# Performance work log

Hardware: AMD Instinct MI355X
Metric: run time of the kernel (lower is better)

## Reference

```python
import jax, jax.numpy as jnp
import numpy as np

TQ, T, D = 2048, 16384, 256
H, KD, VD, DOUT = 8, 32, 32, 256


def setup_inputs() -> dict:
    key = jax.random.key(0)
    ks = jax.random.split(key, 8)
    w_scale = 1.0 / np.sqrt(D)
    return {
        "query": jax.random.normal(ks[0], (TQ, D), dtype=jnp.float32),
        "key": jax.random.normal(ks[1], (T, D), dtype=jnp.float32),
        "value": jax.random.normal(ks[2], (T, D), dtype=jnp.float32),
        "wq": jax.random.normal(ks[3], (D, H * KD), dtype=jnp.float32) * w_scale,
        "bq": jnp.zeros((H * KD,), dtype=jnp.float32),
        "wk": jax.random.normal(ks[4], (D, H * KD), dtype=jnp.float32) * w_scale,
        "bk": jnp.zeros((H * KD,), dtype=jnp.float32),
        "wv": jax.random.normal(ks[5], (D, H * VD), dtype=jnp.float32) * w_scale,
        "bv": jnp.zeros((H * VD,), dtype=jnp.float32),
        "wo": jax.random.normal(ks[6], (H * VD, DOUT), dtype=jnp.float32) * (1.0 / np.sqrt(H * VD)),
        "bo": jnp.zeros((DOUT,), dtype=jnp.float32),
    }


def reference(query, key, value, wq, bq, wk, bk, wv, bv, wo, bo):
    # Linear projections to heads: [Tq,H,KD], [T,H,KD], [T,H,VD]
    qh = (query @ wq + bq).reshape(TQ, H, KD)
    kh = (key @ wk + bk).reshape(T, H, KD)
    vh = (value @ wv + bv).reshape(T, H, VD)
    # Chunked online-softmax attention == exact softmax attention.
    # Query scaled by 1/sqrt(head_dim) as in the memory-efficient impl.
    scale = np.float32(1.0 / np.sqrt(KD))
    logits = jnp.einsum("qhd,khd->hqk", qh * scale, kh)  # [H,Tq,T]
    weights = jax.nn.softmax(logits, axis=-1)
    attn = jnp.einsum("hqk,khd->qhd", weights, vh).reshape(TQ, H * VD)
    return attn @ wo + bo  # [Tq, DOUT]
```

## Files before the change

### kernel.cpp

```cpp
#include <hip/hip_runtime.h>
#include <stdint.h>


typedef float f32x4 __attribute__((ext_vector_type(4)));
typedef __bf16 bf16x8 __attribute__((ext_vector_type(8)));

__device__ __forceinline__ unsigned short f2bf(float f) {
  unsigned int u = __builtin_bit_cast(unsigned int, f);
  u += 0x7FFFu + ((u >> 16) & 1u);
  return (unsigned short)(u >> 16);
}
__device__ __forceinline__ float bf2f(unsigned u) {
  return __builtin_bit_cast(float, u << 16);
}
__device__ __forceinline__ f32x4 mfma16(bf16x8 a, bf16x8 b, f32x4 c) {
  return __builtin_amdgcn_mfma_f32_16x16x32_bf16(a, b, c, 0, 0, 0);
}
__device__ __forceinline__ float ex2(float x) {
#if __has_builtin(__builtin_amdgcn_exp2f)
  return __builtin_amdgcn_exp2f(x);
#else
  return exp2f(x);
#endif
}
__device__ __forceinline__ uint2 pack4(f32x4 a) {
  uint2 r;
  r.x = (unsigned)f2bf(a[0]) | ((unsigned)f2bf(a[1]) << 16);
  r.y = (unsigned)f2bf(a[2]) | ((unsigned)f2bf(a[3]) << 16);
  return r;
}

#define QSCALE 0.25503483f

__global__ __launch_bounds__(256) void convert_w_kernel(
    const float* __restrict__ wq, const float* __restrict__ wk,
    const float* __restrict__ wv, const float* __restrict__ wo,
    unsigned short* __restrict__ tq, unsigned short* __restrict__ tk,
    unsigned short* __restrict__ tv, unsigned short* __restrict__ to)
{
  const int mat = blockIdx.x >> 6, k0 = (blockIdx.x & 63) * 4, n = threadIdx.x;
  const float* src; unsigned short* dst;
  if (mat == 0) { src = wq; dst = tq; }
  else if (mat == 1) { src = wk; dst = tk; }
  else if (mat == 2) { src = wv; dst = tv; }
  else { src = wo; dst = to; }
  unsigned e0 = f2bf(src[(size_t)(k0 + 0) * 256 + n]);
  unsigned e1 = f2bf(src[(size_t)(k0 + 1) * 256 + n]);
  unsigned e2 = f2bf(src[(size_t)(k0 + 2) * 256 + n]);
  unsigned e3 = f2bf(src[(size_t)(k0 + 3) * 256 + n]);
  uint2 pk = { e0 | (e1 << 16), e2 | (e3 << 16) };
  *(uint2*)&dst[(size_t)n * 256 + k0] = pk;
}

__global__ __launch_bounds__(512) void proj4_kernel(
    const float* __restrict__ Xq, const float* __restrict__ Xk,
    const float* __restrict__ Xv,
    const unsigned short* __restrict__ Wtq, const unsigned short* __restrict__ Wtk,
    const unsigned short* __restrict__ Wtv,
    const float* __restrict__ Bq, const float* __restrict__ Bk,
    const float* __restrict__ Bv,
    unsigned short* __restrict__ Oq, unsigned short* __restrict__ Ok,
    unsigned short* __restrict__ Ov)
{
  const int mat = blockIdx.y;
  const float* X; const unsigned short* Wt; const float* Bp; unsigned short* Op;
  int N; float scale; int vmode;
  if (mat == 0) {
    if (blockIdx.x >= 32) return;
    X = Xq; Wt = Wtq; Bp = Bq; Op = Oq; N = 2048; scale = QSCALE; vmode = 0;
  } else if (mat == 1) {
    X = Xk; Wt = Wtk; Bp = Bk; Op = Ok; N = 16384; scale = 1.f; vmode = 0;
  } else {
    X = Xv; Wt = Wtv; Bp = Bv; Op = Ov; N = 16384; scale = 1.f; vmode = 1;
  }
  const int tid = threadIdx.x;
  const int w = tid >> 6, lane = tid & 63, g = lane >> 4, c = lane & 15;
  const int m0 = blockIdx.x * 64;

  __shared__ __align__(16) unsigned short Xs[64 * 40];
  __shared__ __align__(16) unsigned short Ws[256 * 40];

  const f32x4 zero4 = {0.f, 0.f, 0.f, 0.f};
  f32x4 acc[4][2];
  #pragma unroll
  for (int i = 0; i < 4; ++i) { acc[i][0] = zero4; acc[i][1] = zero4; }

  const int xrow = tid >> 3, xseg = (tid & 7) * 4;
  const int wrow = tid >> 1, wseg = (tid & 1) * 16;

  for (int k0 = 0; k0 < 256; k0 += 32) {
    if (k0) __syncthreads();
    {
      float4 x = *(const float4*)&X[(size_t)(m0 + xrow) * 256 + k0 + xseg];
      uint2 px = { (unsigned)f2bf(x.x) | ((unsigned)f2bf(x.y) << 16),
                   (unsigned)f2bf(x.z) | ((unsigned)f2bf(x.w) << 16) };
      *(uint2*)&Xs[xrow * 40 + xseg] = px;
    }
    {
      const unsigned short* wp = Wt + (size_t)wrow * 256 + k0 + wseg;
      int4 w0 = *(const int4*)wp;
      int4 w1 = *(const int4*)(wp + 8);
      *(int4*)&Ws[wrow * 40 + wseg] = w0;
      *(int4*)&Ws[wrow * 40 + wseg + 8] = w1;
    }
    __syncthreads();

    bf16x8 a[4], b[2];
    #pragma unroll
    for (int rt = 0; rt < 4; ++rt)
      a[rt] = *(const bf16x8*)&Xs[(16 * rt + c) * 40 + 8 * g];
    #pragma unroll
    for (int ct = 0; ct < 2; ++ct)
      b[ct] = *(const bf16x8*)&Ws[(32 * w + 16 * ct + c) * 40 + 8 * g];
    #pragma unroll
    for (int rt = 0; rt < 4; ++rt)
      #pragma unroll
      for (int ct = 0; ct < 2; ++ct)
        acc[rt][ct] = mfma16(a[rt], b[ct], acc[rt][ct]);
  }

  #pragma unroll
  for (int ct = 0; ct < 2; ++ct) {
    const int col = 32 * w + 16 * ct + c;
    const float bv = Bp[col];
    const int hh = col >> 5, d = col & 31;
    #pragma unroll
    for (int rt = 0; rt < 4; ++rt)
      #pragma unroll
      for (int r = 0; r < 4; ++r) {
        const int row = m0 + 16 * rt + 4 * g + r;
        const unsigned short v = f2bf((acc[rt][ct][r] + bv) * scale);
        if (vmode) {
          const int pr = (row & ~31) | (((row >> 3) & 1) << 4) |
                         (((row >> 2) & 1) << 3) | (((row >> 4) & 1) << 2) |
                         (row & 3);
          Op[((size_t)hh * 32 + d) * (size_t)N + pr] = v;
        } else {
          Op[((size_t)hh * N + row) * 32 + d] = v;
        }
      }
  }
}

__global__ __launch_bounds__(256) void attn4_kernel(
    const unsigned short* __restrict__ qh, const unsigned short* __restrict__ kh,
    const unsigned short* __restrict__ vth,
    unsigned short* __restrict__ part_o, float* __restrict__ part_l)
{
  const int f = blockIdx.x + 16 * (blockIdx.y + 8 * blockIdx.z);
  const int v = (f & 7) * 128 + (f >> 3);
  const int qb = v & 15, h = (v >> 4) & 7, sp = v >> 7;

  const int tid = threadIdx.x;
  const int w = tid >> 6, lane = tid & 63, g = lane >> 4, c = lane & 15;
  const int q0 = qb * 128 + w * 32;

  __shared__ __align__(16) unsigned short Ks[2][64 * 40];
  __shared__ __align__(16) unsigned short Vt[2][32 * 72];

  const bf16x8 qf0 = *(const bf16x8*)&qh[((size_t)h * 2048 + q0 + c) * 32 + 8 * g];
  const bf16x8 qf1 = *(const bf16x8*)&qh[((size_t)h * 2048 + q0 + 16 + c) * 32 + 8 * g];

  const f32x4 zero4 = {0.f, 0.f, 0.f, 0.f};
  f32x4 acc00 = zero4, acc01 = zero4, acc10 = zero4, acc11 = zero4;
  float l0 = 0.f, l1 = 0.f;

  const int skey = tid >> 2, sseg = (tid & 3) * 8;
  const int kwoff = skey * 40 + sseg;
  const int vrow = tid >> 3, vseg = (tid & 7) * 8;
  const int vwoff = vrow * 72 + vseg;

  const unsigned short* kp = kh + (size_t)h * 524288 +
                             ((size_t)(sp * 2048) + skey) * 32 + sseg;
  const unsigned short* vp = vth + ((size_t)h * 32 + vrow) * 16384 +
                             sp * 2048 + vseg;

  int4 kA = *(const int4*)kp;
  int4 vA = *(const int4*)vp;
  *(int4*)&Ks[0][kwoff] = kA;
  *(int4*)&Vt[0][vwoff] = vA;
  kA = *(const int4*)(kp + 2048);
  vA = *(const int4*)(vp + 64);
  __syncthreads();

  for (int it = 0; it < 32; ++it) {
    const int cur = it & 1;
    if (it < 31) {
      *(int4*)&Ks[cur ^ 1][kwoff] = kA;
      *(int4*)&Vt[cur ^ 1][vwoff] = vA;
      const int t2 = (it + 2) & 31;
      kA = *(const int4*)(kp + t2 * 2048);
      vA = *(const int4*)(vp + t2 * 64);
    }

    const unsigned short* Kb = &Ks[cur][0];
    const unsigned short* Vb = &Vt[cur][0];
    bf16x8 kf0 = *(const bf16x8*)&Kb[(c) * 40 + 8 * g];
    bf16x8 kf1 = *(const bf16x8*)&Kb[(16 + c) * 40 + 8 * g];
    bf16x8 kf2 = *(const bf16x8*)&Kb[(32 + c) * 40 + 8 * g];
    bf16x8 kf3 = *(const bf16x8*)&Kb[(48 + c) * 40 + 8 * g];

    f32x4 s0 = mfma16(kf0, qf0, zero4);
    f32x4 s1 = mfma16(kf1, qf0, zero4);
    f32x4 s2 = mfma16(kf2, qf0, zero4);
    f32x4 s3 = mfma16(kf3, qf0, zero4);
    union { __bf16 b[8]; bf16x8 v; } pa00, pa01, pa10, pa11;
    float rs0 = 0.f;
    #pragma unroll
    for (int r = 0; r < 4; ++r) {
      float p0 = ex2(s0[r]), p1 = ex2(s1[r]);
      float p2 = ex2(s2[r]), p3 = ex2(s3[r]);
      rs0 += (p0 + p1) + (p2 + p3);
      pa00.b[r] = (__bf16)p0; pa00.b[4 + r] = (__bf16)p1;
      pa01.b[r] = (__bf16)p2; pa01.b[4 + r] = (__bf16)p3;
    }
    rs0 += __shfl_xor(rs0, 16);
    rs0 += __shfl_xor(rs0, 32);
    l0 += rs0;
    s0 = mfma16(kf0, qf1, zero4);
    s1 = mfma16(kf1, qf1, zero4);
    s2 = mfma16(kf2, qf1, zero4);
    s3 = mfma16(kf3, qf1, zero4);
    float rs1 = 0.f;
    #pragma unroll
    for (int r = 0; r < 4; ++r) {
      float p0 = ex2(s0[r]), p1 = ex2(s1[r]);
      float p2 = ex2(s2[r]), p3 = ex2(s3[r]);
      rs1 += (p0 + p1) + (p2 + p3);
      pa10.b[r] = (__bf16)p0; pa10.b[4 + r] = (__bf16)p1;
      pa11.b[r] = (__bf16)p2; pa11.b[4 + r] = (__bf16)p3;
    }
    rs1 += __shfl_xor(rs1, 16);
    rs1 += __shfl_xor(rs1, 32);
    l1 += rs1;

    bf16x8 v00 = *(const bf16x8*)&Vb[c * 72 + 8 * g];
    bf16x8 v01 = *(const bf16x8*)&Vb[c * 72 + 32 + 8 * g];
    bf16x8 v10 = *(const bf16x8*)&Vb[(16 + c) * 72 + 8 * g];
    bf16x8 v11 = *(const bf16x8*)&Vb[(16 + c) * 72 + 32 + 8 * g];
    __builtin_amdgcn_s_setprio(1);
    acc00 = mfma16(v00, pa00.v, acc00);
    acc01 = mfma16(v10, pa00.v, acc01);
    acc00 = mfma16(v01, pa01.v, acc00);
    acc01 = mfma16(v11, pa01.v, acc01);
    acc10 = mfma16(v00, pa10.v, acc10);
    acc11 = mfma16(v10, pa10.v, acc11);
    acc10 = mfma16(v01, pa11.v, acc10);
    acc11 = mfma16(v11, pa11.v, acc11);
    __builtin_amdgcn_s_setprio(0);

    __syncthreads();
  }

  const size_t pbase = (size_t)(sp * 8 + h) * 2048;
  unsigned short* po0 = part_o + (pbase + q0 + c) * 32;
  *(uint2*)&po0[4 * g]      = pack4(acc00);
  *(uint2*)&po0[16 + 4 * g] = pack4(acc01);
  unsigned short* po1 = part_o + (pbase + q0 + 16 + c) * 32;
  *(uint2*)&po1[4 * g]      = pack4(acc10);
  *(uint2*)&po1[16 + 4 * g] = pack4(acc11);
  if (lane < 16) {
    part_l[pbase + q0 + lane]      = l0;
    part_l[pbase + q0 + 16 + lane] = l1;
  }
}

__global__ __launch_bounds__(512) void oproj4_kernel(
    const unsigned short* __restrict__ part_o, const float* __restrict__ part_l,
    const unsigned short* __restrict__ Wt, const float* __restrict__ bias,
    float* __restrict__ out)
{
  const int tid = threadIdx.x;
  const int w = tid >> 6, lane = tid & 63, g = lane >> 4, c = lane & 15;
  const int m0 = blockIdx.x * 64;

  __shared__ __align__(16) unsigned short As[64 * 40];
  __shared__ __align__(16) unsigned short Ws[256 * 40];

  const f32x4 zero4 = {0.f, 0.f, 0.f, 0.f};
  f32x4 acc[4][2];
  #pragma unroll
  for (int i = 0; i < 4; ++i) { acc[i][0] = zero4; acc[i][1] = zero4; }

  const int arow = tid >> 3, aseg = (tid & 7) * 4;
  const int wrow = tid >> 1, wseg = (tid & 1) * 16;

  for (int k0 = 0; k0 < 256; k0 += 32) {
    const int h = k0 >> 5;
    if (k0) __syncthreads();
    {
      float L = 0.f;
      float o0 = 0.f, o1 = 0.f, o2 = 0.f, o3 = 0.f;
      #pragma unroll
      for (int s = 0; s < 8; ++s) {
        const size_t b = (size_t)(s * 8 + h) * 2048 + m0 + arow;
        L += part_l[b];
        uint2 pk = *(const uint2*)&part_o[b * 32 + aseg];
        o0 += bf2f(pk.x & 0xffffu); o1 += bf2f(pk.x >> 16);
        o2 += bf2f(pk.y & 0xffffu); o3 += bf2f(pk.y >> 16);
      }
      const float inv = 1.f / L;
      uint2 pa = { (unsigned)f2bf(o0 * inv) | ((unsigned)f2bf(o1 * inv) << 16),
                   (unsigned)f2bf(o2 * inv) | ((unsigned)f2bf(o3 * inv) << 16) };
      *(uint2*)&As[arow * 40 + aseg] = pa;
    }
    {
      const unsigned short* wp = Wt + (size_t)wrow * 256 + k0 + wseg;
      int4 w0 = *(const int4*)wp;
      int4 w1 = *(const int4*)(wp + 8);
      *(int4*)&Ws[wrow * 40 + wseg] = w0;
      *(int4*)&Ws[wrow * 40 + wseg + 8] = w1;
    }
    __syncthreads();

    bf16x8 a[4], b[2];
    #pragma unroll
    for (int rt = 0; rt < 4; ++rt)
      a[rt] = *(const bf16x8*)&As[(16 * rt + c) * 40 + 8 * g];
    #pragma unroll
    for (int ct = 0; ct < 2; ++ct)
      b[ct] = *(const bf16x8*)&Ws[(32 * w + 16 * ct + c) * 40 + 8 * g];
    #pragma unroll
    for (int rt = 0; rt < 4; ++rt)
      #pragma unroll
      for (int ct = 0; ct < 2; ++ct)
        acc[rt][ct] = mfma16(a[rt], b[ct], acc[rt][ct]);
  }

  #pragma unroll
  for (int ct = 0; ct < 2; ++ct) {
    const int col = 32 * w + 16 * ct + c;
    const float bv = bias[col];
    #pragma unroll
    for (int rt = 0; rt < 4; ++rt)
      #pragma unroll
      for (int r = 0; r < 4; ++r)
        out[(size_t)(m0 + 16 * rt + 4 * g + r) * 256 + col] = acc[rt][ct][r] + bv;
  }
}

extern "C" void kernel_launch(void* const* d_in, const int* in_sizes, int n_in,
                              void* d_out, int out_size, void* d_ws, size_t ws_size,
                              hipStream_t stream)
{
  (void)in_sizes; (void)n_in; (void)out_size; (void)ws_size;
  const float* query = (const float*)d_in[0];
  const float* key   = (const float*)d_in[1];
  const float* value = (const float*)d_in[2];
  const float* wq    = (const float*)d_in[3];
  const float* bq    = (const float*)d_in[4];
  const float* wk    = (const float*)d_in[5];
  const float* bk    = (const float*)d_in[6];
  const float* wv    = (const float*)d_in[7];
  const float* bv    = (const float*)d_in[8];
  const float* wo    = (const float*)d_in[9];
  const float* bo    = (const float*)d_in[10];
  float* out = (float*)d_out;

  unsigned char* ws = (unsigned char*)d_ws;
  unsigned short* qh     = (unsigned short*)(ws);
  unsigned short* khp    = (unsigned short*)(ws + 1048576);
  unsigned short* vtp    = (unsigned short*)(ws + 9437184);
  unsigned short* part_o = (unsigned short*)(ws + 17825792);
  unsigned short* wtq    = (unsigned short*)(ws + 17825792);
  unsigned short* wtk    = (unsigned short*)(ws + 17956864);
  unsigned short* wtv    = (unsigned short*)(ws + 18087936);
  float*          part_l = (float*)(ws + 26214400);
  unsigned short* wto    = (unsigned short*)(ws + 26738688);

  convert_w_kernel<<<256, 256, 0, stream>>>(wq, wk, wv, wo, wtq, wtk, wtv, wto);
  proj4_kernel<<<dim3(256, 3), 512, 0, stream>>>(
      query, key, value, wtq, wtk, wtv, bq, bk, bv, qh, khp, vtp);
  attn4_kernel<<<dim3(16, 8, 8), 256, 0, stream>>>(qh, khp, vtp, part_o, part_l);
  oproj4_kernel<<<32, 512, 0, stream>>>(part_o, part_l, wto, bo, out);
}
```

Measured before the change: 111.6 us.

## Compute softmax row sums on MFMA, unroll double buffer, widen oproj grid

The attention kernel now gets the softmax denominators from extra MFMAs against a ones vector instead of VALU adds and cross-lane shuffles. It also uses hardware bf16 conversion packed in pairs and unrolls the double-buffered loop by two with separate shared buffers, which removes the dynamic buffer indexing. The output projection now uses 16-row tiles over 128 blocks of 256 threads instead of 32 blocks, to fill more compute units. The trade-offs are extra MFMA issue slots in the attention loop and reloading the weight matrix in more blocks.

```diff
diff --git a/kernel.cpp b/kernel.cpp
--- a/kernel.cpp
+++ b/kernel.cpp
@@ -22,6 +22,11 @@
 #else
   return exp2f(x);
 #endif
+}
+__device__ __forceinline__ unsigned pk2(float a, float b) {
+  unsigned short ua = __builtin_bit_cast(unsigned short, (__bf16)a);
+  unsigned short ub = __builtin_bit_cast(unsigned short, (__bf16)b);
+  return (unsigned)ua | ((unsigned)ub << 16);
 }
 __device__ __forceinline__ uint2 pack4(f32x4 a) {
   uint2 r;
@@ -92,8 +97,7 @@
     if (k0) __syncthreads();
     {
       float4 x = *(const float4*)&X[(size_t)(m0 + xrow) * 256 + k0 + xseg];
-      uint2 px = { (unsigned)f2bf(x.x) | ((unsigned)f2bf(x.y) << 16),
-                   (unsigned)f2bf(x.z) | ((unsigned)f2bf(x.w) << 16) };
+      uint2 px = { pk2(x.x, x.y), pk2(x.z, x.w) };
       *(uint2*)&Xs[xrow * 40 + xseg] = px;
     }
     {
@@ -142,7 +146,7 @@
   }
 }
 
-__global__ __launch_bounds__(256) void attn4_kernel(
+__global__ __launch_bounds__(256) void attn5_kernel(
     const unsigned short* __restrict__ qh, const unsigned short* __restrict__ kh,
     const unsigned short* __restrict__ vth,
     unsigned short* __restrict__ part_o, float* __restrict__ part_l)
@@ -155,15 +159,19 @@
   const int w = tid >> 6, lane = tid & 63, g = lane >> 4, c = lane & 15;
   const int q0 = qb * 128 + w * 32;
 
-  __shared__ __align__(16) unsigned short Ks[2][64 * 40];
-  __shared__ __align__(16) unsigned short Vt[2][32 * 72];
+  __shared__ __align__(16) unsigned short Ks0[64 * 40], Ks1[64 * 40];
+  __shared__ __align__(16) unsigned short Vt0[32 * 72], Vt1[32 * 72];
 
   const bf16x8 qf0 = *(const bf16x8*)&qh[((size_t)h * 2048 + q0 + c) * 32 + 8 * g];
   const bf16x8 qf1 = *(const bf16x8*)&qh[((size_t)h * 2048 + q0 + 16 + c) * 32 + 8 * g];
 
+  bf16x8 ones;
+  #pragma unroll
+  for (int j = 0; j < 8; ++j) ones[j] = (__bf16)1.0f;
+
   const f32x4 zero4 = {0.f, 0.f, 0.f, 0.f};
   f32x4 acc00 = zero4, acc01 = zero4, acc10 = zero4, acc11 = zero4;
-  float l0 = 0.f, l1 = 0.f;
+  f32x4 accL0 = zero4, accL1 = zero4;
 
   const int skey = tid >> 2, sseg = (tid & 3) * 8;
   const int kwoff = skey * 40 + sseg;
@@ -175,64 +183,37 @@
   const unsigned short* vp = vth + ((size_t)h * 32 + vrow) * 16384 +
                              sp * 2048 + vseg;
 
-  int4 kA = *(const int4*)kp;
-  int4 vA = *(const int4*)vp;
-  *(int4*)&Ks[0][kwoff] = kA;
-  *(int4*)&Vt[0][vwoff] = vA;
-  kA = *(const int4*)(kp + 2048);
-  vA = *(const int4*)(vp + 64);
-  __syncthreads();
-
-  for (int it = 0; it < 32; ++it) {
-    const int cur = it & 1;
-    if (it < 31) {
-      *(int4*)&Ks[cur ^ 1][kwoff] = kA;
-      *(int4*)&Vt[cur ^ 1][vwoff] = vA;
-      const int t2 = (it + 2) & 31;
-      kA = *(const int4*)(kp + t2 * 2048);
-      vA = *(const int4*)(vp + t2 * 64);
-    }
-
-    const unsigned short* Kb = &Ks[cur][0];
-    const unsigned short* Vb = &Vt[cur][0];
+  auto compute = [&](const unsigned short* Kb, const unsigned short* Vb) {
     bf16x8 kf0 = *(const bf16x8*)&Kb[(c) * 40 + 8 * g];
     bf16x8 kf1 = *(const bf16x8*)&Kb[(16 + c) * 40 + 8 * g];
     bf16x8 kf2 = *(const bf16x8*)&Kb[(32 + c) * 40 + 8 * g];
     bf16x8 kf3 = *(const bf16x8*)&Kb[(48 + c) * 40 + 8 * g];
-
     f32x4 s0 = mfma16(kf0, qf0, zero4);
     f32x4 s1 = mfma16(kf1, qf0, zero4);
     f32x4 s2 = mfma16(kf2, qf0, zero4);
     f32x4 s3 = mfma16(kf3, qf0, zero4);
-    union { __bf16 b[8]; bf16x8 v; } pa00, pa01, pa10, pa11;
-    float rs0 = 0.f;
-    #pragma unroll
-    for (int r = 0; r < 4; ++r) {
-      float p0 = ex2(s0[r]), p1 = ex2(s1[r]);
-      float p2 = ex2(s2[r]), p3 = ex2(s3[r]);
-      rs0 += (p0 + p1) + (p2 + p3);
-      pa00.b[r] = (__bf16)p0; pa00.b[4 + r] = (__bf16)p1;
-      pa01.b[r] = (__bf16)p2; pa01.b[4 + r] = (__bf16)p3;
-    }
-    rs0 += __shfl_xor(rs0, 16);
-    rs0 += __shfl_xor(rs0, 32);
-    l0 += rs0;
-    s0 = mfma16(kf0, qf1, zero4);
-    s1 = mfma16(kf1, qf1, zero4);
-    s2 = mfma16(kf2, qf1, zero4);
-    s3 = mfma16(kf3, qf1, zero4);
-    float rs1 = 0.f;
-    #pragma unroll
-    for (int r = 0; r < 4; ++r) {
-      float p0 = ex2(s0[r]), p1 = ex2(s1[r]);
-      float p2 = ex2(s2[r]), p3 = ex2(s3[r]);
-      rs1 += (p0 + p1) + (p2 + p3);
-      pa10.b[r] = (__bf16)p0; pa10.b[4 + r] = (__bf16)p1;
-      pa11.b[r] = (__bf16)p2; pa11.b[4 + r] = (__bf16)p3;
-    }
-    rs1 += __shfl_xor(rs1, 16);
-    rs1 += __shfl_xor(rs1, 32);
-    l1 += rs1;
+    f32x4 t0 = mfma16(kf0, qf1, zero4);
+    f32x4 t1 = mfma16(kf1, qf1, zero4);
+    f32x4 t2 = mfma16(kf2, qf1, zero4);
+    f32x4 t3 = mfma16(kf3, qf1, zero4);
+
+    union { unsigned u[4]; bf16x8 v; } pa00, pa01, pa10, pa11;
+    pa00.u[0] = pk2(ex2(s0[0]), ex2(s0[1]));
+    pa00.u[1] = pk2(ex2(s0[2]), ex2(s0[3]));
+    pa00.u[2] = pk2(ex2(s1[0]), ex2(s1[1]));
+    pa00.u[3] = pk2(ex2(s1[2]), ex2(s1[3]));
+    pa01.u[0] = pk2(ex2(s2[0]), ex2(s2[1]));
+    pa01.u[1] = pk2(ex2(s2[2]), ex2(s2[3]));
+    pa01.u[2] = pk2(ex2(s3[0]), ex2(s3[1]));
+    pa01.u[3] = pk2(ex2(s3[2]), ex2(s3[3]));
+    pa10.u[0] = pk2(ex2(t0[0]), ex2(t0[1]));
+    pa10.u[1] = pk2(ex2(t0[2]), ex2(t0[3]));
+    pa10.u[2] = pk2(ex2(t1[0]), ex2(t1[1]));
+    pa10.u[3] = pk2(ex2(t1[2]), ex2(t1[3]));
+    pa11.u[0] = pk2(ex2(t2[0]), ex2(t2[1]));
+    pa11.u[1] = pk2(ex2(t2[2]), ex2(t2[3]));
+    pa11.u[2] = pk2(ex2(t3[0]), ex2(t3[1]));
+    pa11.u[3] = pk2(ex2(t3[2]), ex2(t3[3]));
 
     bf16x8 v00 = *(const bf16x8*)&Vb[c * 72 + 8 * g];
     bf16x8 v01 = *(const bf16x8*)&Vb[c * 72 + 32 + 8 * g];
@@ -241,14 +222,48 @@
     __builtin_amdgcn_s_setprio(1);
     acc00 = mfma16(v00, pa00.v, acc00);
     acc01 = mfma16(v10, pa00.v, acc01);
+    accL0 = mfma16(ones, pa00.v, accL0);
     acc00 = mfma16(v01, pa01.v, acc00);
     acc01 = mfma16(v11, pa01.v, acc01);
+    accL0 = mfma16(ones, pa01.v, accL0);
     acc10 = mfma16(v00, pa10.v, acc10);
     acc11 = mfma16(v10, pa10.v, acc11);
+    accL1 = mfma16(ones, pa10.v, accL1);
     acc10 = mfma16(v01, pa11.v, acc10);
     acc11 = mfma16(v11, pa11.v, acc11);
+    accL1 = mfma16(ones, pa11.v, accL1);
     __builtin_amdgcn_s_setprio(0);
-
+  };
+
+  {
+    int4 k0r = *(const int4*)kp;
+    int4 v0r = *(const int4*)vp;
+    *(int4*)&Ks0[kwoff] = k0r;
+    *(int4*)&Vt0[vwoff] = v0r;
+  }
+  int4 kr = *(const int4*)(kp + 2048);
+  int4 vr = *(const int4*)(vp + 64);
+  __syncthreads();
+
+  for (int i2 = 0; i2 < 16; ++i2) {
+    const int it = i2 * 2;
+    *(int4*)&Ks1[kwoff] = kr;
+    *(int4*)&Vt1[vwoff] = vr;
+    {
+      const int t = (it + 2) & 31;
+      kr = *(const int4*)(kp + t * 2048);
+      vr = *(const int4*)(vp + t * 64);
+    }
+    compute(Ks0, Vt0);
+    __syncthreads();
+    *(int4*)&Ks0[kwoff] = kr;
+    *(int4*)&Vt0[vwoff] = vr;
+    {
+      const int t = (it + 3) & 31;
+      kr = *(const int4*)(kp + t * 2048);
+      vr = *(const int4*)(vp + t * 64);
+    }
+    compute(Ks1, Vt1);
     __syncthreads();
   }
 
@@ -260,82 +275,74 @@
   *(uint2*)&po1[4 * g]      = pack4(acc10);
   *(uint2*)&po1[16 + 4 * g] = pack4(acc11);
   if (lane < 16) {
-    part_l[pbase + q0 + lane]      = l0;
-    part_l[pbase + q0 + 16 + lane] = l1;
-  }
-}
-
-__global__ __launch_bounds__(512) void oproj4_kernel(
+    part_l[pbase + q0 + lane]      = accL0[0];
+    part_l[pbase + q0 + 16 + lane] = accL1[0];
+  }
+}
+
+__global__ __launch_bounds__(256) void oproj5_kernel(
     const unsigned short* __restrict__ part_o, const float* __restrict__ part_l,
     const unsigned short* __restrict__ Wt, const float* __restrict__ bias,
     float* __restrict__ out)
 {
   const int tid = threadIdx.x;
   const int w = tid >> 6, lane = tid & 63, g = lane >> 4, c = lane & 15;
-  const int m0 = blockIdx.x * 64;
-
-  __shared__ __align__(16) unsigned short As[64 * 40];
+  const int m0 = blockIdx.x * 16;
+
+  __shared__ __align__(16) unsigned short As[16 * 40];
   __shared__ __align__(16) unsigned short Ws[256 * 40];
 
   const f32x4 zero4 = {0.f, 0.f, 0.f, 0.f};
-  f32x4 acc[4][2];
-  #pragma unroll
-  for (int i = 0; i < 4; ++i) { acc[i][0] = zero4; acc[i][1] = zero4; }
-
-  const int arow = tid >> 3, aseg = (tid & 7) * 4;
-  const int wrow = tid >> 1, wseg = (tid & 1) * 16;
+  f32x4 acc[4];
+  #pragma unroll
+  for (int i = 0; i < 4; ++i) acc[i] = zero4;
+
+  const int arow = tid >> 4, ad = (tid & 15) * 2;
 
   for (int k0 = 0; k0 < 256; k0 += 32) {
     const int h = k0 >> 5;
     if (k0) __syncthreads();
     {
-      float L = 0.f;
-      float o0 = 0.f, o1 = 0.f, o2 = 0.f, o3 = 0.f;
+      float L = 0.f, o0 = 0.f, o1 = 0.f;
       #pragma unroll
       for (int s = 0; s < 8; ++s) {
         const size_t b = (size_t)(s * 8 + h) * 2048 + m0 + arow;
         L += part_l[b];
-        uint2 pk = *(const uint2*)&part_o[b * 32 + aseg];
-        o0 += bf2f(pk.x & 0xffffu); o1 += bf2f(pk.x >> 16);
-        o2 += bf2f(pk.y & 0xffffu); o3 += bf2f(pk.y >> 16);
+        const unsigned pk = *(const unsigned*)&part_o[b * 32 + ad];
+        o0 += bf2f(pk & 0xffffu);
+        o1 += bf2f(pk >> 16);
       }
       const float inv = 1.f / L;
-      uint2 pa = { (unsigned)f2bf(o0 * inv) | ((unsigned)f2bf(o1 * inv) << 16),
-                   (unsigned)f2bf(o2 * inv) | ((unsigned)f2bf(o3 * inv) << 16) };
-      *(uint2*)&As[arow * 40 + aseg] = pa;
-    }
-    {
-      const unsigned short* wp = Wt + (size_t)wrow * 256 + k0 + wseg;
+      *(unsigned*)&As[arow * 40 + ad] = pk2(o0 * inv, o1 * inv);
+    }
+    {
+      const unsigned short* wp = Wt + (size_t)tid * 256 + k0;
       int4 w0 = *(const int4*)wp;
       int4 w1 = *(const int4*)(wp + 8);
-      *(int4*)&Ws[wrow * 40 + wseg] = w0;
-      *(int4*)&Ws[wrow * 40 + wseg + 8] = w1;
+      int4 w2 = *(const int4*)(wp + 16);
+      int4 w3 = *(const int4*)(wp + 24);
+      *(int4*)&Ws[tid * 40 + 0]  = w0;
+      *(int4*)&Ws[tid * 40 + 8]  = w1;
+      *(int4*)&Ws[tid * 40 + 16] = w2;
+      *(int4*)&Ws[tid * 40 + 24] = w3;
     }
     __syncthreads();
 
-    bf16x8 a[4], b[2];
-    #pragma unroll
-    for (int rt = 0; rt < 4; ++rt)
-      a[rt] = *(const bf16x8*)&As[(16 * rt + c) * 40 + 8 * g];
-    #pragma unroll
-    for (int ct = 0; ct < 2; ++ct)
-      b[ct] = *(const bf16x8*)&Ws[(32 * w + 16 * ct + c) * 40 + 8 * g];
-    #pragma unroll
-    for (int rt = 0; rt < 4; ++rt)
-      #pragma unroll
-      for (int ct = 0; ct < 2; ++ct)
-        acc[rt][ct] = mfma16(a[rt], b[ct], acc[rt][ct]);
-  }
-
-  #pragma unroll
-  for (int ct = 0; ct < 2; ++ct) {
-    const int col = 32 * w + 16 * ct + c;
+    bf16x8 a = *(const bf16x8*)&As[c * 40 + 8 * g];
+    #pragma unroll
+    for (int ct = 0; ct < 4; ++ct) {
+      bf16x8 b = *(const bf16x8*)&Ws[(64 * w + 16 * ct + c) * 40 + 8 * g];
+      acc[ct] = mfma16(a, b, acc[ct]);
+    }
+  }
+
+  #pragma unroll
+  for (int ct = 0; ct < 4; ++ct) {
+    const int col = 64 * w + 16 * ct + c;
     const float bv = bias[col];
     #pragma unroll
-    for (int rt = 0; rt < 4; ++rt)
-      #pragma unroll
-      for (int r = 0; r < 4; ++r)
-        out[(size_t)(m0 + 16 * rt + 4 * g + r) * 256 + col] = acc[rt][ct][r] + bv;
+    for (int r = 0; r < 4; ++r)
+      out[(size_t)(m0 + 4 * g + r) * 256 + col] = acc[ct][r] + bv;
   }
 }
 
@@ -371,6 +378,6 @@
   convert_w_kernel<<<256, 256, 0, stream>>>(wq, wk, wv, wo, wtq, wtk, wtv, wto);
   proj4_kernel<<<dim3(256, 3), 512, 0, stream>>>(
       query, key, value, wtq, wtk, wtv, bq, bk, bv, qh, khp, vtp);
-  attn4_kernel<<<dim3(16, 8, 8), 256, 0, stream>>>(qh, khp, vtp, part_o, part_l);
-  oproj4_kernel<<<32, 512, 0, stream>>>(part_o, part_l, wto, bo, out);
-}
+  attn5_kernel<<<dim3(16, 8, 8), 256, 0, stream>>>(qh, khp, vtp, part_o, part_l);
+  oproj5_kernel<<<128, 256, 0, stream>>>(part_o, part_l, wto, bo, out);
+}
```

Result: slower. 130.4 us (+16.9%).
